# Kernel optimization log

Hardware: AMD Instinct MI355X
Metric: run time of the kernel (lower is better)

The kernel has to match this reference:

```python
import jax, jax.numpy as jnp
import numpy as np

N, K, D, VOCAB = 20000, 32, 128, 100000
NEG = -1e30  # finite large-negative so all-masked rows don't produce NaN softmax


def setup_inputs() -> dict:
    key = jax.random.key(0)
    ks = jax.random.split(key, 10)
    return {
        "nodes": jax.random.randint(ks[0], (N,), 0, VOCAB),
        "neigh_idx": jax.random.randint(ks[1], (N, K), 0, VOCAB),
        "neigh_len": jax.random.randint(ks[2], (N,), 0, K + 1),
        "u2e": jax.random.normal(ks[3], (VOCAB, D), dtype=jnp.float32),
        "W1": jax.random.normal(ks[4], (D, 2 * D), dtype=jnp.float32) * 0.05,
        "b1": jax.random.normal(ks[5], (D,), dtype=jnp.float32) * 0.05,
        "W2": jax.random.normal(ks[6], (D, D), dtype=jnp.float32) * 0.05,
        "b2": jax.random.normal(ks[7], (D,), dtype=jnp.float32) * 0.05,
        "W3": jax.random.normal(ks[8], (1, D), dtype=jnp.float32) * 0.05,
        "b3": jax.random.normal(ks[9], (1,), dtype=jnp.float32) * 0.05,
    }


def reference(nodes, neigh_idx, neigh_len, u2e, W1, b1, W2, b2, W3, b3):
    # self features: [N, D]
    self_feats = u2e[nodes]
    # neighbor features gather: [N, K, D]
    e_u = u2e[neigh_idx]
    # GraphRec Attention: cat(neighbor, self-broadcast) -> MLP -> softmax over K
    x = jnp.concatenate(
        [e_u, jnp.broadcast_to(self_feats[:, None, :], e_u.shape)], axis=-1
    )  # [N, K, 2D]
    h = jax.nn.relu(jnp.einsum("nkf,df->nkd", x, W1) + b1)
    h = jax.nn.relu(jnp.einsum("nkd,ed->nke", h, W2) + b2)
    logits = jnp.einsum("nkd,od->nko", h, W3)[..., 0] + b3[0]  # [N, K]
    mask = jnp.arange(K)[None, :] < neigh_len[:, None]  # [N, K]
    att = jax.nn.softmax(jnp.where(mask, logits, NEG), axis=1)
    att = jnp.where(mask, att, 0.0)  # zero out padded slots (and all-empty rows)
    # attention-weighted neighbor aggregation: [N, D]
    agg = jnp.einsum("nk,nkd->nd", att, e_u)
    has_neigh = (neigh_len > 0)[:, None]
    return jnp.where(has_neigh, (agg + self_feats) * 0.5, self_feats)
```

## Files before the change

### kernel.cpp

```cpp
#include <hip/hip_runtime.h>
#include <hip/hip_bf16.h>
#include <stdint.h>

#define KN 32
#define D  128
#define NNODES 20000
#define GRID 2500
#define ITERS 4

typedef __bf16 bf16;
typedef __bf16 bf16x8 __attribute__((ext_vector_type(8)));
typedef float  f32x4  __attribute__((ext_vector_type(4)));

#define CHUNK_DW 260
#define EU_NODE_DW (16 * CHUNK_DW)
#define H_STRIDE 136

#define GL2LDS(src, dst) __builtin_amdgcn_global_load_lds(                 \
    (const __attribute__((address_space(1))) void*)(src),                  \
    (__attribute__((address_space(3))) void*)(dst), 16, 0, 0)

#define MFMA(a, b, c) __builtin_amdgcn_mfma_f32_16x16x32_bf16((a), (b), (c), 0, 0, 0)

__global__ __launch_bounds__(256) void pack_weights_kernel(
    const float* __restrict__ W1, const float* __restrict__ W2,
    bf16* __restrict__ w1p, bf16* __restrict__ w2p)
{
    int t = blockIdx.x * 256 + threadIdx.x;
    if (t < 32768) {
        int j = t & 7, lane = (t >> 3) & 63, kt = (t >> 9) & 7, nt = t >> 12;
        int d = nt * 16 + (lane & 15);
        int f = kt * 32 + ((lane >> 4) << 3) + j;
        w1p[t] = (bf16)W1[d * 256 + f];
    } else if (t < 49152) {
        int u = t - 32768;
        int j = u & 7, lane = (u >> 3) & 63, kt = (u >> 9) & 3, nt = u >> 11;
        int e  = nt * 16 + (lane & 15);
        int dd = kt * 32 + ((lane >> 4) << 3) + j;
        w2p[u] = (bf16)W2[e * 128 + dd];
    }
}

__global__ __launch_bounds__(256, 3) void graphrec_agg_kernel(
    const int*   __restrict__ nodes,
    const int*   __restrict__ neigh_idx,
    const int*   __restrict__ neigh_len,
    const float* __restrict__ u2e,
    const float* __restrict__ b1,
    const float* __restrict__ b2,
    const float* __restrict__ W3,
    const float* __restrict__ b3,
    const bf16*  __restrict__ w1p,
    const bf16*  __restrict__ w2p,
    float*       __restrict__ out)
{
    __shared__ alignas(16) float eu[2 * EU_NODE_DW];
    __shared__ alignas(16) bf16  h1[2 * KN * H_STRIDE];
    __shared__ alignas(16) float self_f[2 * D];
    __shared__ float lpart[2][4 * KN];
    __shared__ float att_s[2][KN];

    const int t    = threadIdx.x;
    const int lane = t & 63;
    const int wave = t >> 6;
    const int ln15 = lane & 15;
    const int quad = lane >> 4;
    const int nt0  = wave * 2;

    const float bias1_0 = b1[nt0 * 16 + ln15];
    const float bias1_1 = b1[(nt0 + 1) * 16 + ln15];
    const float bias2_0 = b2[nt0 * 16 + ln15];
    const float bias2_1 = b2[(nt0 + 1) * 16 + ln15];
    const float w3_0    = W3[nt0 * 16 + ln15];
    const float w3_1    = W3[(nt0 + 1) * 16 + ln15];
    const float b3v     = b3[0];

    bf16x8 w1r[2][8];
    #pragma unroll
    for (int nt = 0; nt < 2; ++nt)
        #pragma unroll
        for (int ft = 0; ft < 8; ++ft)
            w1r[nt][ft] = *(const bf16x8*)(w1p + ((nt0 + nt) * 8 + ft) * 512 + lane * 8);
    bf16x8 w2r[2][4];
    #pragma unroll
    for (int nt = 0; nt < 2; ++nt)
        #pragma unroll
        for (int kt = 0; kt < 4; ++kt)
            w2r[nt][kt] = *(const bf16x8*)(w2p + ((nt0 + nt) * 4 + kt) * 512 + lane * 8);

    #pragma unroll 1
    for (int it = 0; it < ITERS; ++it) {
        const int nA   = blockIdx.x * 8 + it * 2;
        const int lenA = neigh_len[nA];
        const int lenB = neigh_len[nA + 1];

        {
            const int half = lane >> 5;
            const int colb = (lane & 31) << 4;
            #pragma unroll
            for (int nd = 0; nd < 2; ++nd) {
                #pragma unroll
                for (int j = 0; j < 4; ++j) {
                    int chunk = wave * 4 + j;
                    int idx = neigh_idx[(nA + nd) * KN + chunk + (half << 4)];
                    const char* src = (const char*)(u2e + (size_t)idx * D) + colb;
                    GL2LDS(src, eu + nd * EU_NODE_DW + chunk * CHUNK_DW);
                }
            }
            if (wave == 0) {
                int sidx = nodes[nA + half];
                const char* src = (const char*)(u2e + (size_t)sidx * D) + colb;
                GL2LDS(src, self_f);
            }
        }
        __syncthreads();

        #pragma unroll 1
        for (int nd = 0; nd < 2; ++nd) {
            const float* euN = eu + nd * EU_NODE_DW;
            const float* sfN = self_f + nd * D;
            bf16* h1N = h1 + nd * KN * H_STRIDE;

            f32x4 c00 = {0.f,0.f,0.f,0.f}, c01 = c00, c10 = c00, c11 = c00;
            const int r0 = ln15 * CHUNK_DW;
            #pragma unroll
            for (int ft = 0; ft < 4; ++ft) {
                int off = ft * 32 + quad * 8;
                f32x4 u0 = *(const f32x4*)(euN + r0 + off);
                f32x4 u1 = *(const f32x4*)(euN + r0 + off + 4);
                f32x4 v0 = *(const f32x4*)(euN + r0 + 128 + off);
                f32x4 v1 = *(const f32x4*)(euN + r0 + 128 + off + 4);
                bf16x8 a0, a1;
                #pragma unroll
                for (int e = 0; e < 4; ++e) {
                    a0[e] = (bf16)u0[e]; a0[4 + e] = (bf16)u1[e];
                    a1[e] = (bf16)v0[e]; a1[4 + e] = (bf16)v1[e];
                }
                c00 = MFMA(a0, w1r[0][ft], c00);
                c01 = MFMA(a0, w1r[1][ft], c01);
                c10 = MFMA(a1, w1r[0][ft], c10);
                c11 = MFMA(a1, w1r[1][ft], c11);
            }
            #pragma unroll
            for (int ft = 4; ft < 8; ++ft) {
                int off = (ft - 4) * 32 + quad * 8;
                f32x4 u0 = *(const f32x4*)(sfN + off);
                f32x4 u1 = *(const f32x4*)(sfN + off + 4);
                bf16x8 a;
                #pragma unroll
                for (int e = 0; e < 4; ++e) { a[e] = (bf16)u0[e]; a[4 + e] = (bf16)u1[e]; }
                c00 = MFMA(a, w1r[0][ft], c00);
                c01 = MFMA(a, w1r[1][ft], c01);
                c10 = MFMA(a, w1r[0][ft], c10);
                c11 = MFMA(a, w1r[1][ft], c11);
            }
            #pragma unroll
            for (int r = 0; r < 4; ++r) {
                int row = quad * 4 + r;
                h1N[row * H_STRIDE + nt0 * 16 + ln15]              = (bf16)fmaxf(c00[r] + bias1_0, 0.f);
                h1N[row * H_STRIDE + (nt0 + 1) * 16 + ln15]        = (bf16)fmaxf(c01[r] + bias1_1, 0.f);
                h1N[(16 + row) * H_STRIDE + nt0 * 16 + ln15]       = (bf16)fmaxf(c10[r] + bias1_0, 0.f);
                h1N[(16 + row) * H_STRIDE + (nt0 + 1) * 16 + ln15] = (bf16)fmaxf(c11[r] + bias1_1, 0.f);
            }
        }
        __syncthreads();

        #pragma unroll 1
        for (int nd = 0; nd < 2; ++nd) {
            const bf16* h1N = h1 + nd * KN * H_STRIDE;
            f32x4 d00 = {0.f,0.f,0.f,0.f}, d01 = d00, d10 = d00, d11 = d00;
            #pragma unroll
            for (int kt = 0; kt < 4; ++kt) {
                bf16x8 a0 = *(const bf16x8*)(h1N + ln15 * H_STRIDE + kt * 32 + quad * 8);
                bf16x8 a1 = *(const bf16x8*)(h1N + (16 + ln15) * H_STRIDE + kt * 32 + quad * 8);
                d00 = MFMA(a0, w2r[0][kt], d00);
                d01 = MFMA(a0, w2r[1][kt], d01);
                d10 = MFMA(a1, w2r[0][kt], d10);
                d11 = MFMA(a1, w2r[1][kt], d11);
            }
            #pragma unroll
            for (int r = 0; r < 4; ++r) {
                float p0 = w3_0 * fmaxf(d00[r] + bias2_0, 0.f)
                         + w3_1 * fmaxf(d01[r] + bias2_1, 0.f);
                float p1 = w3_0 * fmaxf(d10[r] + bias2_0, 0.f)
                         + w3_1 * fmaxf(d11[r] + bias2_1, 0.f);
                #pragma unroll
                for (int o = 1; o < 16; o <<= 1) {
                    p0 += __shfl_xor(p0, o);
                    p1 += __shfl_xor(p1, o);
                }
                if (ln15 == 0) {
                    lpart[nd][wave * KN + quad * 4 + r]      = p0;
                    lpart[nd][wave * KN + 16 + quad * 4 + r] = p1;
                }
            }
        }
        __syncthreads();

        if (wave < 2) {
            int nd = wave, k = lane & 31;
            float lg = lpart[nd][k] + lpart[nd][KN + k] + lpart[nd][2 * KN + k]
                     + lpart[nd][3 * KN + k] + b3v;
            int len = nd ? lenB : lenA;
            bool act = (lane < 32) && (k < len);
            float l = act ? lg : -1e30f;
            float m = l;
            #pragma unroll
            for (int o = 1; o < 32; o <<= 1) m = fmaxf(m, __shfl_xor(m, o));
            float e = act ? expf(l - m) : 0.f;
            float s = e;
            #pragma unroll
            for (int o = 1; o < 32; o <<= 1) s += __shfl_xor(s, o);
            if (lane < 32) att_s[nd][k] = (s > 0.f) ? (e / s) : 0.f;
        }
        __syncthreads();

        {
            int nd = t >> 7, d = t & 127;
            const float* euN = eu + nd * EU_NODE_DW;
            float acc = 0.f;
            #pragma unroll
            for (int k = 0; k < KN; ++k)
                acc += att_s[nd][k] * euN[(k & 15) * CHUNK_DW + ((k >> 4) << 7) + d];
            float sf = self_f[nd * D + d];
            int len = nd ? lenB : lenA;
            out[(size_t)(nA + nd) * D + d] = (len > 0) ? 0.5f * (acc + sf) : sf;
        }
        __syncthreads();
    }
}

extern "C" void kernel_launch(void* const* d_in, const int* in_sizes, int n_in,
                              void* d_out, int out_size, void* d_ws, size_t ws_size,
                              hipStream_t stream) {
    const int*   nodes     = (const int*)d_in[0];
    const int*   neigh_idx = (const int*)d_in[1];
    const int*   neigh_len = (const int*)d_in[2];
    const float* u2e       = (const float*)d_in[3];
    const float* W1        = (const float*)d_in[4];
    const float* b1        = (const float*)d_in[5];
    const float* W2        = (const float*)d_in[6];
    const float* b2        = (const float*)d_in[7];
    const float* W3        = (const float*)d_in[8];
    const float* b3        = (const float*)d_in[9];
    float* out = (float*)d_out;

    bf16* w1p = (bf16*)d_ws;
    bf16* w2p = w1p + 32768;

    pack_weights_kernel<<<192, 256, 0, stream>>>(W1, W2, w1p, w2p);
    graphrec_agg_kernel<<<GRID, 256, 0, stream>>>(nodes, neigh_idx, neigh_len, u2e,
                                                  b1, b2, W3, b3, w1p, w2p, out);
}
```

Before: 233.3 us.

## Gather from bf16 table copy with double-buffered LDS prefetch and fused softmax

Adds a per-call kernel that converts the embedding table to bf16 in workspace. The main kernel then gathers neighbor rows from that copy, halving gather bytes and removing in-loop conversions. Gathers for the next node pair are issued into a second LDS buffer while the current pair is computed, and neighbor indices are loaded two steps ahead. Softmax and weighted aggregation are merged into one phase using shuffles, and some barriers become lighter LDS-only waits. In exchange, every call streams the whole table for conversion, and the aggregation now uses bf16 neighbor values, which adds rounding error. If the workspace is too small, the original kernel runs as a fallback.

```diff
diff --git a/kernel.cpp b/kernel.cpp
--- a/kernel.cpp
+++ b/kernel.cpp
@@ -7,13 +7,14 @@
 #define NNODES 20000
 #define GRID 2500
 #define ITERS 4
+#define VOCAB 100000
 
 typedef __bf16 bf16;
 typedef __bf16 bf16x8 __attribute__((ext_vector_type(8)));
 typedef float  f32x4  __attribute__((ext_vector_type(4)));
 
-#define CHUNK_DW 260
-#define EU_NODE_DW (16 * CHUNK_DW)
+#define CHUNK_E 520
+#define EU_NODE_E (8 * CHUNK_E)
 #define H_STRIDE 136
 
 #define GL2LDS(src, dst) __builtin_amdgcn_global_load_lds(                 \
@@ -21,6 +22,12 @@
     (__attribute__((address_space(3))) void*)(dst), 16, 0, 0)
 
 #define MFMA(a, b, c) __builtin_amdgcn_mfma_f32_16x16x32_bf16((a), (b), (c), 0, 0, 0)
+
+__device__ __forceinline__ void bar_lds() {
+    asm volatile("s_waitcnt lgkmcnt(0)" ::: "memory");
+    __builtin_amdgcn_s_barrier();
+    asm volatile("" ::: "memory");
+}
 
 __global__ __launch_bounds__(256) void pack_weights_kernel(
     const float* __restrict__ W1, const float* __restrict__ W2,
@@ -41,7 +48,219 @@
     }
 }
 
+__global__ __launch_bounds__(256) void convert_table_kernel(
+    const float* __restrict__ u2e, bf16* __restrict__ tbl)
+{
+    size_t i = ((size_t)blockIdx.x * 256 + threadIdx.x) * 8;
+    float4 a = *(const float4*)(u2e + i);
+    float4 b = *(const float4*)(u2e + i + 4);
+    bf16x8 v;
+    v[0]=(bf16)a.x; v[1]=(bf16)a.y; v[2]=(bf16)a.z; v[3]=(bf16)a.w;
+    v[4]=(bf16)b.x; v[5]=(bf16)b.y; v[6]=(bf16)b.z; v[7]=(bf16)b.w;
+    *(bf16x8*)(tbl + i) = v;
+}
+
+
+#define ISSUE_GATHER(EU, SF)                                                    \
+    {                                                                           \
+        _Pragma("unroll")                                                       \
+        for (int j = 0; j < 4; ++j)                                             \
+            GL2LDS(u2e_bf + (size_t)gidx[j] * D + ((lane & 15) << 3),           \
+                   (EU) + gnd * EU_NODE_E + (cbase + j) * CHUNK_E);             \
+        if (wave == 0)                                                          \
+            GL2LDS(u2e + (size_t)sidx * D + ((lane & 31) << 2), (SF));          \
+    }
+
+#define LOAD_IDX(NP)                                                            \
+    {                                                                           \
+        int nb_ = blockIdx.x * 8 + (NP) * 2;                                    \
+        _Pragma("unroll")                                                       \
+        for (int j = 0; j < 4; ++j)                                             \
+            gidx[j] = neigh_idx[(nb_ + gnd) * KN + cbase + j + ((lane >> 4) << 3)]; \
+        if (wave == 0) sidx = nodes[nb_ + (lane >> 5)];                         \
+    }
+
+#define STEP(IT, CEU, CSF, NEU, NSF)                                            \
+    {                                                                           \
+        const int nA   = blockIdx.x * 8 + (IT) * 2;                             \
+        const int lenA = neigh_len[nA];                                         \
+        const int lenB = neigh_len[nA + 1];                                     \
+        if ((IT) < ITERS - 1) ISSUE_GATHER(NEU, NSF);                           \
+        { int np_ = ((IT) + 2 < ITERS) ? (IT) + 2 : ITERS - 1; LOAD_IDX(np_); } \
+                                                         \
+        _Pragma("unroll 1")                                                     \
+        for (int nd = 0; nd < 2; ++nd) {                                        \
+            const bf16*  euN = (CEU) + nd * EU_NODE_E;                          \
+            const float* sfN = (CSF) + nd * D;                                  \
+            bf16* h1N = h1 + nd * KN * H_STRIDE;                                \
+            f32x4 c00 = {0.f,0.f,0.f,0.f}, c01 = c00, c10 = c00, c11 = c00;     \
+            const int rb = (ln15 & 7) * CHUNK_E + (ln15 >> 3) * 128;            \
+            _Pragma("unroll")                                                   \
+            for (int ft = 0; ft < 4; ++ft) {                                    \
+                bf16x8 a0 = *(const bf16x8*)(euN + rb + ft * 32 + quad * 8);    \
+                bf16x8 a1 = *(const bf16x8*)(euN + rb + 256 + ft * 32 + quad * 8); \
+                c00 = MFMA(a0, w1r[0][ft], c00);                                \
+                c01 = MFMA(a0, w1r[1][ft], c01);                                \
+                c10 = MFMA(a1, w1r[0][ft], c10);                                \
+                c11 = MFMA(a1, w1r[1][ft], c11);                                \
+            }                                                                   \
+            _Pragma("unroll")                                                   \
+            for (int ft = 4; ft < 8; ++ft) {                                    \
+                int off = (ft - 4) * 32 + quad * 8;                             \
+                f32x4 u0 = *(const f32x4*)(sfN + off);                          \
+                f32x4 u1 = *(const f32x4*)(sfN + off + 4);                      \
+                bf16x8 a;                                                       \
+                _Pragma("unroll")                                               \
+                for (int e = 0; e < 4; ++e) { a[e] = (bf16)u0[e]; a[4+e] = (bf16)u1[e]; } \
+                c00 = MFMA(a, w1r[0][ft], c00);                                 \
+                c01 = MFMA(a, w1r[1][ft], c01);                                 \
+                c10 = MFMA(a, w1r[0][ft], c10);                                 \
+                c11 = MFMA(a, w1r[1][ft], c11);                                 \
+            }                                                                   \
+            _Pragma("unroll")                                                   \
+            for (int r = 0; r < 4; ++r) {                                       \
+                int row = quad * 4 + r;                                         \
+                h1N[row * H_STRIDE + nt0 * 16 + ln15]              = (bf16)fmaxf(c00[r] + bias1_0, 0.f); \
+                h1N[row * H_STRIDE + (nt0 + 1) * 16 + ln15]        = (bf16)fmaxf(c01[r] + bias1_1, 0.f); \
+                h1N[(16 + row) * H_STRIDE + nt0 * 16 + ln15]       = (bf16)fmaxf(c10[r] + bias1_0, 0.f); \
+                h1N[(16 + row) * H_STRIDE + (nt0 + 1) * 16 + ln15] = (bf16)fmaxf(c11[r] + bias1_1, 0.f); \
+            }                                                                   \
+        }                                                                       \
+        bar_lds();                                                              \
+                                          \
+        _Pragma("unroll 1")                                                     \
+        for (int nd = 0; nd < 2; ++nd) {                                        \
+            const bf16* h1N = h1 + nd * KN * H_STRIDE;                          \
+            f32x4 d00 = {0.f,0.f,0.f,0.f}, d01 = d00, d10 = d00, d11 = d00;     \
+            _Pragma("unroll")                                                   \
+            for (int kt = 0; kt < 4; ++kt) {                                    \
+                bf16x8 a0 = *(const bf16x8*)(h1N + ln15 * H_STRIDE + kt * 32 + quad * 8); \
+                bf16x8 a1 = *(const bf16x8*)(h1N + (16 + ln15) * H_STRIDE + kt * 32 + quad * 8); \
+                d00 = MFMA(a0, w2r[0][kt], d00);                                \
+                d01 = MFMA(a0, w2r[1][kt], d01);                                \
+                d10 = MFMA(a1, w2r[0][kt], d10);                                \
+                d11 = MFMA(a1, w2r[1][kt], d11);                                \
+            }                                                                   \
+            _Pragma("unroll")                                                   \
+            for (int r = 0; r < 4; ++r) {                                       \
+                float p0 = w3_0 * fmaxf(d00[r] + bias2_0, 0.f)                  \
+                         + w3_1 * fmaxf(d01[r] + bias2_1, 0.f);                 \
+                float p1 = w3_0 * fmaxf(d10[r] + bias2_0, 0.f)                  \
+                         + w3_1 * fmaxf(d11[r] + bias2_1, 0.f);                 \
+                _Pragma("unroll")                                               \
+                for (int o = 1; o < 16; o <<= 1) {                              \
+                    p0 += __shfl_xor(p0, o);                                    \
+                    p1 += __shfl_xor(p1, o);                                    \
+                }                                                               \
+                if (ln15 == 0) {                                                \
+                    lpart[nd][wave * KN + quad * 4 + r]      = p0;              \
+                    lpart[nd][wave * KN + 16 + quad * 4 + r] = p1;              \
+                }                                                               \
+            }                                                                   \
+        }                                                                       \
+        bar_lds();                                                              \
+          \
+        {                                                                       \
+            int nd  = wave >> 1;                                                \
+            int d   = ((wave & 1) << 6) + lane;                                 \
+            int k   = lane & 31;                                                \
+            float lg = lpart[nd][k] + lpart[nd][32 + k] + lpart[nd][64 + k]     \
+                     + lpart[nd][96 + k] + b3v;                                 \
+            int len = nd ? lenB : lenA;                                         \
+            bool act = k < len;                                                 \
+            float l = act ? lg : -1e30f;                                        \
+            float m = l;                                                        \
+            _Pragma("unroll")                                                   \
+            for (int o = 1; o < 32; o <<= 1) m = fmaxf(m, __shfl_xor(m, o));    \
+            float e = act ? expf(l - m) : 0.f;                                  \
+            float s = e;                                                        \
+            _Pragma("unroll")                                                   \
+            for (int o = 1; o < 32; o <<= 1) s += __shfl_xor(s, o);             \
+            float att = (s > 0.f) ? (e / s) : 0.f;                              \
+            const bf16* euN = (CEU) + nd * EU_NODE_E;                           \
+            float acc = 0.f;                                                    \
+            _Pragma("unroll")                                                   \
+            for (int k2 = 0; k2 < KN; ++k2) {                                   \
+                float a  = __shfl(att, k2);                                     \
+                float ev = (float)euN[(k2 & 7) * CHUNK_E + (k2 >> 3) * 128 + d]; \
+                acc += a * ev;                                                  \
+            }                                                                   \
+            float sf = (CSF)[nd * D + d];                                       \
+            out[(size_t)(nA + nd) * D + d] = (len > 0) ? 0.5f * (acc + sf) : sf; \
+        }                                                                       \
+        __syncthreads();  \
+    }
+
 __global__ __launch_bounds__(256, 3) void graphrec_agg_kernel(
+    const int*   __restrict__ nodes,
+    const int*   __restrict__ neigh_idx,
+    const int*   __restrict__ neigh_len,
+    const float* __restrict__ u2e,
+    const bf16*  __restrict__ u2e_bf,
+    const float* __restrict__ b1,
+    const float* __restrict__ b2,
+    const float* __restrict__ W3,
+    const float* __restrict__ b3,
+    const bf16*  __restrict__ w1p,
+    const bf16*  __restrict__ w2p,
+    float*       __restrict__ out)
+{
+    __shared__ alignas(16) bf16  eu0[2 * EU_NODE_E];
+    __shared__ alignas(16) bf16  eu1[2 * EU_NODE_E];
+    __shared__ alignas(16) float sf0[2 * D];
+    __shared__ alignas(16) float sf1[2 * D];
+    __shared__ alignas(16) bf16  h1[2 * KN * H_STRIDE];
+    __shared__ float lpart[2][4 * KN];
+
+    const int t     = threadIdx.x;
+    const int lane  = t & 63;
+    const int wave  = t >> 6;
+    const int ln15  = lane & 15;
+    const int quad  = lane >> 4;
+    const int nt0   = wave * 2;
+    const int gnd   = wave >> 1;
+    const int cbase = (wave & 1) * 4;
+
+    const float bias1_0 = b1[nt0 * 16 + ln15];
+    const float bias1_1 = b1[(nt0 + 1) * 16 + ln15];
+    const float bias2_0 = b2[nt0 * 16 + ln15];
+    const float bias2_1 = b2[(nt0 + 1) * 16 + ln15];
+    const float w3_0    = W3[nt0 * 16 + ln15];
+    const float w3_1    = W3[(nt0 + 1) * 16 + ln15];
+    const float b3v     = b3[0];
+
+    bf16x8 w1r[2][8];
+    #pragma unroll
+    for (int nt = 0; nt < 2; ++nt)
+        #pragma unroll
+        for (int ft = 0; ft < 8; ++ft)
+            w1r[nt][ft] = *(const bf16x8*)(w1p + ((nt0 + nt) * 8 + ft) * 512 + lane * 8);
+    bf16x8 w2r[2][4];
+    #pragma unroll
+    for (int nt = 0; nt < 2; ++nt)
+        #pragma unroll
+        for (int kt = 0; kt < 4; ++kt)
+            w2r[nt][kt] = *(const bf16x8*)(w2p + ((nt0 + nt) * 4 + kt) * 512 + lane * 8);
+
+    int gidx[4];
+    int sidx = 0;
+
+    LOAD_IDX(0);
+    ISSUE_GATHER(eu0, sf0);
+    LOAD_IDX(1);
+    __syncthreads();
+
+    #pragma unroll 1
+    for (int hi = 0; hi < ITERS; hi += 2) {
+        STEP(hi,     eu0, sf0, eu1, sf1);
+        STEP(hi + 1, eu1, sf1, eu0, sf0);
+    }
+}
+
+#define FB_CHUNK_DW 260
+#define FB_EU_NODE_DW (16 * FB_CHUNK_DW)
+
+__global__ __launch_bounds__(256, 3) void graphrec_agg_fb(
     const int*   __restrict__ nodes,
     const int*   __restrict__ neigh_idx,
     const int*   __restrict__ neigh_len,
@@ -54,7 +273,7 @@
     const bf16*  __restrict__ w2p,
     float*       __restrict__ out)
 {
-    __shared__ alignas(16) float eu[2 * EU_NODE_DW];
+    __shared__ alignas(16) float eu[2 * FB_EU_NODE_DW];
     __shared__ alignas(16) bf16  h1[2 * KN * H_STRIDE];
     __shared__ alignas(16) float self_f[2 * D];
     __shared__ float lpart[2][4 * KN];
@@ -93,7 +312,6 @@
         const int nA   = blockIdx.x * 8 + it * 2;
         const int lenA = neigh_len[nA];
         const int lenB = neigh_len[nA + 1];
-
         {
             const int half = lane >> 5;
             const int colb = (lane & 31) << 4;
@@ -104,7 +322,7 @@
                     int chunk = wave * 4 + j;
                     int idx = neigh_idx[(nA + nd) * KN + chunk + (half << 4)];
                     const char* src = (const char*)(u2e + (size_t)idx * D) + colb;
-                    GL2LDS(src, eu + nd * EU_NODE_DW + chunk * CHUNK_DW);
+                    GL2LDS(src, eu + nd * FB_EU_NODE_DW + chunk * FB_CHUNK_DW);
                 }
             }
             if (wave == 0) {
@@ -114,15 +332,13 @@
             }
         }
         __syncthreads();
-
         #pragma unroll 1
         for (int nd = 0; nd < 2; ++nd) {
-            const float* euN = eu + nd * EU_NODE_DW;
+            const float* euN = eu + nd * FB_EU_NODE_DW;
             const float* sfN = self_f + nd * D;
             bf16* h1N = h1 + nd * KN * H_STRIDE;
-
             f32x4 c00 = {0.f,0.f,0.f,0.f}, c01 = c00, c10 = c00, c11 = c00;
-            const int r0 = ln15 * CHUNK_DW;
+            const int r0 = ln15 * FB_CHUNK_DW;
             #pragma unroll
             for (int ft = 0; ft < 4; ++ft) {
                 int off = ft * 32 + quad * 8;
@@ -164,7 +380,6 @@
             }
         }
         __syncthreads();
-
         #pragma unroll 1
         for (int nd = 0; nd < 2; ++nd) {
             const bf16* h1N = h1 + nd * KN * H_STRIDE;
@@ -196,7 +411,6 @@
             }
         }
         __syncthreads();
-
         if (wave < 2) {
             int nd = wave, k = lane & 31;
             float lg = lpart[nd][k] + lpart[nd][KN + k] + lpart[nd][2 * KN + k]
@@ -214,14 +428,13 @@
             if (lane < 32) att_s[nd][k] = (s > 0.f) ? (e / s) : 0.f;
         }
         __syncthreads();
-
         {
             int nd = t >> 7, d = t & 127;
-            const float* euN = eu + nd * EU_NODE_DW;
+            const float* euN = eu + nd * FB_EU_NODE_DW;
             float acc = 0.f;
             #pragma unroll
             for (int k = 0; k < KN; ++k)
-                acc += att_s[nd][k] * euN[(k & 15) * CHUNK_DW + ((k >> 4) << 7) + d];
+                acc += att_s[nd][k] * euN[(k & 15) * FB_CHUNK_DW + ((k >> 4) << 7) + d];
             float sf = self_f[nd * D + d];
             int len = nd ? lenB : lenA;
             out[(size_t)(nA + nd) * D + d] = (len > 0) ? 0.5f * (acc + sf) : sf;
@@ -247,8 +460,17 @@
 
     bf16* w1p = (bf16*)d_ws;
     bf16* w2p = w1p + 32768;
+    bf16* u2e_bf = (bf16*)((char*)d_ws + 98304);
+    const size_t need = 98304ull + (size_t)VOCAB * D * 2;
 
     pack_weights_kernel<<<192, 256, 0, stream>>>(W1, W2, w1p, w2p);
-    graphrec_agg_kernel<<<GRID, 256, 0, stream>>>(nodes, neigh_idx, neigh_len, u2e,
+    if (ws_size >= need) {
+        convert_table_kernel<<<VOCAB * D / 2048, 256, 0, stream>>>(u2e, u2e_bf);
+        graphrec_agg_kernel<<<GRID, 256, 0, stream>>>(nodes, neigh_idx, neigh_len,
+                                                      u2e, u2e_bf, b1, b2, W3, b3,
+                                                      w1p, w2p, out);
+    } else {
+        graphrec_agg_fb<<<GRID, 256, 0, stream>>>(nodes, neigh_idx, neigh_len, u2e,
                                                   b1, b2, W3, b3, w1p, w2p, out);
-}
+    }
+}
```

Measured after the change: 269.1 us. 1.15x slower.

## Gather neighbor rows from a per-call bf16 copy of the embedding table

Applied to the files above, without the earlier changes.

Adds a kernel that converts the whole fp32 embedding table to bf16 in workspace on every call. The main kernel then gathers 256-byte bf16 neighbor rows directly into LDS, halving the bytes moved by the random gather, which dominates runtime. The main kernel is also reorganised to 512 threads, with each wave owning one 16-column output tile. The cost is a full-table conversion pass each call and bf16 rounding of the neighbor features used in the weighted aggregation. The old fp32 kernel is kept as a fallback when workspace is too small.

```diff
diff --git a/kernel.cpp b/kernel.cpp
--- a/kernel.cpp
+++ b/kernel.cpp
@@ -7,13 +7,14 @@
 #define NNODES 20000
 #define GRID 2500
 #define ITERS 4
+#define VOCAB 100000
 
 typedef __bf16 bf16;
 typedef __bf16 bf16x8 __attribute__((ext_vector_type(8)));
 typedef float  f32x4  __attribute__((ext_vector_type(4)));
 
-#define CHUNK_DW 260
-#define EU_NODE_DW (16 * CHUNK_DW)
+#define CHUNK_E 520
+#define EU_NODE_E (8 * CHUNK_E)
 #define H_STRIDE 136
 
 #define GL2LDS(src, dst) __builtin_amdgcn_global_load_lds(                 \
@@ -41,7 +42,183 @@
     }
 }
 
-__global__ __launch_bounds__(256, 3) void graphrec_agg_kernel(
+__global__ __launch_bounds__(256) void convert_table_kernel(
+    const float* __restrict__ u2e, bf16* __restrict__ tbl)
+{
+    size_t i = ((size_t)blockIdx.x * 256 + threadIdx.x) * 8;
+    float4 a = *(const float4*)(u2e + i);
+    float4 b = *(const float4*)(u2e + i + 4);
+    bf16x8 v;
+    v[0]=(bf16)a.x; v[1]=(bf16)a.y; v[2]=(bf16)a.z; v[3]=(bf16)a.w;
+    v[4]=(bf16)b.x; v[5]=(bf16)b.y; v[6]=(bf16)b.z; v[7]=(bf16)b.w;
+    *(bf16x8*)(tbl + i) = v;
+}
+
+__global__ __launch_bounds__(512, 4) void graphrec_agg_kernel(
+    const int*   __restrict__ nodes,
+    const int*   __restrict__ neigh_idx,
+    const int*   __restrict__ neigh_len,
+    const float* __restrict__ u2e,
+    const bf16*  __restrict__ u2e_bf,
+    const float* __restrict__ b1,
+    const float* __restrict__ b2,
+    const float* __restrict__ W3,
+    const float* __restrict__ b3,
+    const bf16*  __restrict__ w1p,
+    const bf16*  __restrict__ w2p,
+    float*       __restrict__ out)
+{
+    __shared__ alignas(16) bf16  eu[2 * EU_NODE_E];
+    __shared__ alignas(16) float self_f[2 * D];
+    __shared__ alignas(16) bf16  h1[2 * KN * H_STRIDE];
+    __shared__ float lpart[2][8 * KN];
+    __shared__ float att_s[2][KN];
+
+    const int t    = threadIdx.x;
+    const int lane = t & 63;
+    const int wave = t >> 6;
+    const int ln15 = lane & 15;
+    const int quad = lane >> 4;
+    const int nt   = wave;
+
+    const float bias1 = b1[nt * 16 + ln15];
+    const float bias2 = b2[nt * 16 + ln15];
+    const float w3v   = W3[nt * 16 + ln15];
+    const float b3v   = b3[0];
+
+    bf16x8 w1r[8];
+    #pragma unroll
+    for (int ft = 0; ft < 8; ++ft)
+        w1r[ft] = *(const bf16x8*)(w1p + (nt * 8 + ft) * 512 + lane * 8);
+    bf16x8 w2r[4];
+    #pragma unroll
+    for (int kt = 0; kt < 4; ++kt)
+        w2r[kt] = *(const bf16x8*)(w2p + (nt * 4 + kt) * 512 + lane * 8);
+
+    #pragma unroll 1
+    for (int it = 0; it < ITERS; ++it) {
+        const int nA   = blockIdx.x * 8 + it * 2;
+        const int lenA = neigh_len[nA];
+        const int lenB = neigh_len[nA + 1];
+
+        {
+            const int gnd = wave >> 2;
+            const int cb  = (wave & 3) * 2;
+            #pragma unroll
+            for (int j = 0; j < 2; ++j) {
+                int chunk = cb + j;
+                int idx = neigh_idx[(nA + gnd) * KN + chunk + ((lane >> 4) << 3)];
+                GL2LDS(u2e_bf + (size_t)idx * D + ((lane & 15) << 3),
+                       eu + gnd * EU_NODE_E + chunk * CHUNK_E);
+            }
+            if (wave == 0) {
+                int sidx = nodes[nA + (lane >> 5)];
+                GL2LDS(u2e + (size_t)sidx * D + ((lane & 31) << 2), self_f);
+            }
+        }
+        __syncthreads();
+
+        #pragma unroll 1
+        for (int nd = 0; nd < 2; ++nd) {
+            const bf16*  euN = eu + nd * EU_NODE_E;
+            const float* sfN = self_f + nd * D;
+            bf16* h1N = h1 + nd * KN * H_STRIDE;
+
+            f32x4 c0 = {0.f,0.f,0.f,0.f}, c1 = c0;
+            const int rb = (ln15 & 7) * CHUNK_E + (ln15 >> 3) * 128;
+            #pragma unroll
+            for (int ft = 0; ft < 4; ++ft) {
+                bf16x8 a0 = *(const bf16x8*)(euN + rb + ft * 32 + quad * 8);
+                bf16x8 a1 = *(const bf16x8*)(euN + rb + 256 + ft * 32 + quad * 8);
+                c0 = MFMA(a0, w1r[ft], c0);
+                c1 = MFMA(a1, w1r[ft], c1);
+            }
+            #pragma unroll
+            for (int ft = 4; ft < 8; ++ft) {
+                int off = (ft - 4) * 32 + quad * 8;
+                f32x4 u0 = *(const f32x4*)(sfN + off);
+                f32x4 u1 = *(const f32x4*)(sfN + off + 4);
+                bf16x8 a;
+                #pragma unroll
+                for (int e = 0; e < 4; ++e) { a[e] = (bf16)u0[e]; a[4 + e] = (bf16)u1[e]; }
+                c0 = MFMA(a, w1r[ft], c0);
+                c1 = MFMA(a, w1r[ft], c1);
+            }
+            #pragma unroll
+            for (int r = 0; r < 4; ++r) {
+                int row = quad * 4 + r;
+                h1N[row * H_STRIDE + nt * 16 + ln15]        = (bf16)fmaxf(c0[r] + bias1, 0.f);
+                h1N[(16 + row) * H_STRIDE + nt * 16 + ln15] = (bf16)fmaxf(c1[r] + bias1, 0.f);
+            }
+        }
+        __syncthreads();
+
+        #pragma unroll 1
+        for (int nd = 0; nd < 2; ++nd) {
+            const bf16* h1N = h1 + nd * KN * H_STRIDE;
+            f32x4 d0 = {0.f,0.f,0.f,0.f}, d1 = d0;
+            #pragma unroll
+            for (int kt = 0; kt < 4; ++kt) {
+                bf16x8 a0 = *(const bf16x8*)(h1N + ln15 * H_STRIDE + kt * 32 + quad * 8);
+                bf16x8 a1 = *(const bf16x8*)(h1N + (16 + ln15) * H_STRIDE + kt * 32 + quad * 8);
+                d0 = MFMA(a0, w2r[kt], d0);
+                d1 = MFMA(a1, w2r[kt], d1);
+            }
+            #pragma unroll
+            for (int r = 0; r < 4; ++r) {
+                float p0 = w3v * fmaxf(d0[r] + bias2, 0.f);
+                float p1 = w3v * fmaxf(d1[r] + bias2, 0.f);
+                #pragma unroll
+                for (int o = 1; o < 16; o <<= 1) {
+                    p0 += __shfl_xor(p0, o);
+                    p1 += __shfl_xor(p1, o);
+                }
+                if (ln15 == 0) {
+                    lpart[nd][wave * KN + quad * 4 + r]      = p0;
+                    lpart[nd][wave * KN + 16 + quad * 4 + r] = p1;
+                }
+            }
+        }
+        __syncthreads();
+
+        if (wave < 2) {
+            int nd = wave, k = lane & 31;
+            float lg = b3v;
+            #pragma unroll
+            for (int j = 0; j < 8; ++j) lg += lpart[nd][j * KN + k];
+            int len = nd ? lenB : lenA;
+            bool act = (lane < 32) && (k < len);
+            float l = act ? lg : -1e30f;
+            float m = l;
+            #pragma unroll
+            for (int o = 1; o < 32; o <<= 1) m = fmaxf(m, __shfl_xor(m, o));
+            float e = act ? expf(l - m) : 0.f;
+            float s = e;
+            #pragma unroll
+            for (int o = 1; o < 32; o <<= 1) s += __shfl_xor(s, o);
+            if (lane < 32) att_s[nd][k] = (s > 0.f) ? (e / s) : 0.f;
+        }
+        __syncthreads();
+
+        if (t < 256) {
+            int nd = t >> 7, d = t & 127;
+            const bf16* euN = eu + nd * EU_NODE_E;
+            float acc = 0.f;
+            #pragma unroll
+            for (int k = 0; k < KN; ++k)
+                acc += att_s[nd][k] * (float)euN[(k & 7) * CHUNK_E + (k >> 3) * 128 + d];
+            float sf = self_f[nd * D + d];
+            int len = nd ? lenB : lenA;
+            out[(size_t)(nA + nd) * D + d] = (len > 0) ? 0.5f * (acc + sf) : sf;
+        }
+        __syncthreads();
+    }
+}
+
+#define FB_CHUNK_DW 260
+#define FB_EU_NODE_DW (16 * FB_CHUNK_DW)
+
+__global__ __launch_bounds__(256, 3) void graphrec_agg_fb(
     const int*   __restrict__ nodes,
     const int*   __restrict__ neigh_idx,
     const int*   __restrict__ neigh_len,
@@ -54,7 +231,7 @@
     const bf16*  __restrict__ w2p,
     float*       __restrict__ out)
 {
-    __shared__ alignas(16) float eu[2 * EU_NODE_DW];
+    __shared__ alignas(16) float eu[2 * FB_EU_NODE_DW];
     __shared__ alignas(16) bf16  h1[2 * KN * H_STRIDE];
     __shared__ alignas(16) float self_f[2 * D];
     __shared__ float lpart[2][4 * KN];
@@ -93,7 +270,6 @@
         const int nA   = blockIdx.x * 8 + it * 2;
         const int lenA = neigh_len[nA];
         const int lenB = neigh_len[nA + 1];
-
         {
             const int half = lane >> 5;
             const int colb = (lane & 31) << 4;
@@ -104,7 +280,7 @@
                     int chunk = wave * 4 + j;
                     int idx = neigh_idx[(nA + nd) * KN + chunk + (half << 4)];
                     const char* src = (const char*)(u2e + (size_t)idx * D) + colb;
-                    GL2LDS(src, eu + nd * EU_NODE_DW + chunk * CHUNK_DW);
+                    GL2LDS(src, eu + nd * FB_EU_NODE_DW + chunk * FB_CHUNK_DW);
                 }
             }
             if (wave == 0) {
@@ -114,15 +290,13 @@
             }
         }
         __syncthreads();
-
         #pragma unroll 1
         for (int nd = 0; nd < 2; ++nd) {
-            const float* euN = eu + nd * EU_NODE_DW;
+            const float* euN = eu + nd * FB_EU_NODE_DW;
             const float* sfN = self_f + nd * D;
             bf16* h1N = h1 + nd * KN * H_STRIDE;
-
             f32x4 c00 = {0.f,0.f,0.f,0.f}, c01 = c00, c10 = c00, c11 = c00;
-            const int r0 = ln15 * CHUNK_DW;
+            const int r0 = ln15 * FB_CHUNK_DW;
             #pragma unroll
             for (int ft = 0; ft < 4; ++ft) {
                 int off = ft * 32 + quad * 8;
@@ -164,7 +338,6 @@
             }
         }
         __syncthreads();
-
         #pragma unroll 1
         for (int nd = 0; nd < 2; ++nd) {
             const bf16* h1N = h1 + nd * KN * H_STRIDE;
@@ -196,7 +369,6 @@
             }
         }
         __syncthreads();
-
         if (wave < 2) {
             int nd = wave, k = lane & 31;
             float lg = lpart[nd][k] + lpart[nd][KN + k] + lpart[nd][2 * KN + k]
@@ -214,14 +386,13 @@
             if (lane < 32) att_s[nd][k] = (s > 0.f) ? (e / s) : 0.f;
         }
         __syncthreads();
-
         {
             int nd = t >> 7, d = t & 127;
-            const float* euN = eu + nd * EU_NODE_DW;
+            const float* euN = eu + nd * FB_EU_NODE_DW;
             float acc = 0.f;
             #pragma unroll
             for (int k = 0; k < KN; ++k)
-                acc += att_s[nd][k] * euN[(k & 15) * CHUNK_DW + ((k >> 4) << 7) + d];
+                acc += att_s[nd][k] * euN[(k & 15) * FB_CHUNK_DW + ((k >> 4) << 7) + d];
             float sf = self_f[nd * D + d];
             int len = nd ? lenB : lenA;
             out[(size_t)(nA + nd) * D + d] = (len > 0) ? 0.5f * (acc + sf) : sf;
@@ -247,8 +418,17 @@
 
     bf16* w1p = (bf16*)d_ws;
     bf16* w2p = w1p + 32768;
+    bf16* u2e_bf = (bf16*)((char*)d_ws + 98304);
+    const size_t need = 98304ull + (size_t)VOCAB * D * 2;
 
     pack_weights_kernel<<<192, 256, 0, stream>>>(W1, W2, w1p, w2p);
-    graphrec_agg_kernel<<<GRID, 256, 0, stream>>>(nodes, neigh_idx, neigh_len, u2e,
+    if (ws_size >= need) {
+        convert_table_kernel<<<VOCAB * D / 2048, 256, 0, stream>>>(u2e, u2e_bf);
+        graphrec_agg_kernel<<<GRID, 512, 0, stream>>>(nodes, neigh_idx, neigh_len,
+                                                      u2e, u2e_bf, b1, b2, W3, b3,
+                                                      w1p, w2p, out);
+    } else {
+        graphrec_agg_fb<<<GRID, 256, 0, stream>>>(nodes, neigh_idx, neigh_len, u2e,
                                                   b1, b2, W3, b3, w1p, w2p, out);
+    }
 }
```

Result: slower. 259.6 us (+11.3%).
